# Kernel optimization log

Measured on AMD Instinct MI355X. Metric: run time of the kernel, lower is better.

Reference implementation:

```python
import jax, jax.numpy as jnp
import numpy as np

HIDDEN = 512
NUM_HEADS = 8


def setup_inputs() -> dict:
    key = jax.random.key(0)
    ks = jax.random.split(key, 8)
    Tq, Tk, Cq, Ck, H = 1, 65536, 512, 512, HIDDEN
    s = 1.0 / np.sqrt(H)
    return {
        "Q": jax.random.normal(ks[0], (Tq, Cq), jnp.float32),
        "K": jax.random.normal(ks[1], (Tk, Ck), jnp.float32),
        "Wq": jax.random.normal(ks[2], (H, Cq), jnp.float32) * s,
        "bq": jax.random.normal(ks[3], (H,), jnp.float32) * s,
        "Wk": jax.random.normal(ks[4], (H, Ck), jnp.float32) * s,
        "bk": jax.random.normal(ks[5], (H,), jnp.float32) * s,
        "Wout": jax.random.normal(ks[6], (1, NUM_HEADS), jnp.float32) * 0.3,
        "bout": jax.random.normal(ks[7], (1,), jnp.float32) * 0.3,
    }


def reference(Q, K, Wq, bq, Wk, bk, Wout, bout):
    h = NUM_HEADS
    H = Wq.shape[0]
    d = H // h  # per-head dim
    # linear + ReLU projections
    Ql = jax.nn.relu(Q @ Wq.T + bq)          # [1, H]
    Kl = jax.nn.relu(K @ Wk.T + bk)          # [Tk, H]
    # split into heads (T_q == 1 is required by linear_out)
    Qh = Ql.reshape(h, d)                    # [h, d]
    Kh = Kl.reshape(-1, h, d)                # [Tk, h, d]
    # per-head scores, scaled by sqrt(d_head); dropout rate 0 -> identity
    scores = jnp.einsum('hd,thd->th', Qh, Kh) / (d ** 0.5)  # [Tk, h]
    # learned per-head fusion, then softmax over the T_k axis
    logits = scores @ Wout.T + bout          # [Tk, 1]
    return jax.nn.softmax(logits, axis=0)    # [Tk, 1]
```

## Files before the change

kernel.cpp:

```cpp
#include <hip/hip_runtime.h>
#include <hip/hip_fp16.h>

#define CDIM 512
#define ROWS 65536
#define TPW  16

typedef _Float16 half8  __attribute__((ext_vector_type(8)));
typedef __fp16   fp16x2 __attribute__((ext_vector_type(2)));
typedef float    f32x16 __attribute__((ext_vector_type(16)));

__device__ __forceinline__ half8 cvt8(float4 f0, float4 f1) {
    union { fp16x2 h2[4]; half8 h8; } u;
    u.h2[0] = __builtin_amdgcn_cvt_pkrtz(f0.x, f0.y);
    u.h2[1] = __builtin_amdgcn_cvt_pkrtz(f0.z, f0.w);
    u.h2[2] = __builtin_amdgcn_cvt_pkrtz(f1.x, f1.y);
    u.h2[3] = __builtin_amdgcn_cvt_pkrtz(f1.z, f1.w);
    return u.h8;
}

__global__ void qproj_kernel(const float* __restrict__ Q, const float* __restrict__ Wq,
                             const float* __restrict__ bq, const float* __restrict__ Wout,
                             float* __restrict__ v) {
    __shared__ float qs[CDIM];
    const int t = threadIdx.x;
    qs[t] = Q[t]; qs[t + 256] = Q[t + 256];
    __syncthreads();
    const int jj  = t >> 4;
    const int sub = t & 15;
    const int j   = blockIdx.x * 16 + jj;
    const float4* w4 = (const float4*)(Wq + (size_t)j * CDIM + sub * 32);
    const float4* q4 = (const float4*)(qs + sub * 32);
    float s = 0.f;
    #pragma unroll
    for (int i = 0; i < 8; ++i) {
        float4 w = w4[i]; float4 q = q4[i];
        s = fmaf(w.x, q.x, s); s = fmaf(w.y, q.y, s);
        s = fmaf(w.z, q.z, s); s = fmaf(w.w, q.w, s);
    }
    s += __shfl_xor(s, 1); s += __shfl_xor(s, 2);
    s += __shfl_xor(s, 4); s += __shfl_xor(s, 8);
    if (sub == 0) {
        s += bq[j];
        s = fmaxf(s, 0.f);
        v[j] = s * Wout[j >> 6] * 0.125f;
    }
}

__global__ void wkfrag_kernel(const float* __restrict__ Wk, _Float16* __restrict__ Wkf) {
    const int gid = blockIdx.x * 256 + threadIdx.x;
    const int jb  = gid >> 11;
    const int kc  = (gid >> 6) & 31;
    const int l   = gid & 63;
    const int j   = jb * 32 + (l & 31);
    const int k   = kc * 16 + (l >> 5) * 8;
    const float* src = Wk + (size_t)j * CDIM + k;
    float4 f0 = *(const float4*)(src);
    float4 f1 = *(const float4*)(src + 4);
    *(half8*)(Wkf + (size_t)gid * 8) = cvt8(f0, f1);
}

__global__ __launch_bounds__(512, 2) void score_kernel(
    const float* __restrict__ Kmat, const _Float16* __restrict__ Wkf,
    const float* __restrict__ bk, const float* __restrict__ v,
    float* __restrict__ partial2)
{
    __shared__ alignas(16) char fragbuf[2][32768];
    __shared__ float scratch2[2][8][32];

    const int tid  = threadIdx.x;
    const int lane = tid & 63;
    const int wave = tid >> 6;
    const int l31  = lane & 31;
    const int lhi  = lane >> 5;

    const int bid      = blockIdx.x;
    const int cls      = (bid >> 3) & 1;
    const int rowblock = (bid & 7) * 16 + (bid >> 4);
    const int rowbase  = rowblock * (TPW * 32);
    const int jb       = cls * 8 + wave;
    float* pbase = partial2 + (size_t)cls * ROWS;

    half8 B[32];
    const half8* bsrc = (const half8*)Wkf + (size_t)jb * 2048 + lane;
    #pragma unroll
    for (int kc = 0; kc < 32; ++kc) B[kc] = bsrc[kc * 64];
    const int jmy = jb * 32 + l31;
    const float bj = bk[jmy];
    const float vj = v[jmy];

    const int kc0  = wave * 4;
    const int srow = tid & 31;
    const int slhi = (tid >> 5) & 1;
    const int slot = tid & 63;

    {
        const float* g0 = Kmat + (size_t)(rowbase + srow) * CDIM + kc0 * 16 + slhi * 8;
        #pragma unroll
        for (int i = 0; i < 4; ++i) {
            float4 f0 = *(const float4*)(g0 + i * 16);
            float4 f1 = *(const float4*)(g0 + i * 16 + 4);
            *(half8*)(&fragbuf[0][(kc0 + i) * 1024 + slot * 16]) = cvt8(f0, f1);
        }
    }
    __syncthreads();

    for (int t = 0; t < TPW; ++t) {
        const int cur = t & 1;
        const bool pf = (t + 1 < TPW);
        const char* sb = fragbuf[cur];
        char* db = fragbuf[cur ^ 1];
        const float* gt = Kmat + (size_t)(rowbase + (pf ? (t + 1) : t) * 32 + srow) * CDIM
                        + kc0 * 16 + slhi * 8;

        if (t > 0 && tid < 32) {
            const int pt = (t - 1) & 1;
            float s = 0.f;
            #pragma unroll
            for (int w = 0; w < 8; ++w) s += scratch2[pt][w][tid];
            pbase[rowbase + (t - 1) * 32 + tid] = s;
        }

        f32x16 acc0, acc1;
        #pragma unroll
        for (int r = 0; r < 16; ++r) { acc0[r] = 0.f; acc1[r] = 0.f; }

        float4 L0, L1, L2, L3;
        if (pf) {
            L0 = *(const float4*)(gt);
            L1 = *(const float4*)(gt + 4);
            L2 = *(const float4*)(gt + 16);
            L3 = *(const float4*)(gt + 20);
        }
        __builtin_amdgcn_sched_barrier(0);

        #pragma unroll
        for (int kc = 0; kc < 16; kc += 2) {
            half8 a0 = *(const half8*)(sb + kc * 1024 + lane * 16);
            half8 a1 = *(const half8*)(sb + (kc + 1) * 1024 + lane * 16);
            acc0 = __builtin_amdgcn_mfma_f32_32x32x16_f16(a0, B[kc],     acc0, 0, 0, 0);
            acc1 = __builtin_amdgcn_mfma_f32_32x32x16_f16(a1, B[kc + 1], acc1, 0, 0, 0);
        }

        if (pf) {
            *(half8*)(db + (kc0 + 0) * 1024 + slot * 16) = cvt8(L0, L1);
            *(half8*)(db + (kc0 + 1) * 1024 + slot * 16) = cvt8(L2, L3);
            L0 = *(const float4*)(gt + 32);
            L1 = *(const float4*)(gt + 36);
            L2 = *(const float4*)(gt + 48);
            L3 = *(const float4*)(gt + 52);
        }
        __builtin_amdgcn_sched_barrier(0);

        #pragma unroll
        for (int kc = 16; kc < 32; kc += 2) {
            half8 a0 = *(const half8*)(sb + kc * 1024 + lane * 16);
            half8 a1 = *(const half8*)(sb + (kc + 1) * 1024 + lane * 16);
            acc0 = __builtin_amdgcn_mfma_f32_32x32x16_f16(a0, B[kc],     acc0, 0, 0, 0);
            acc1 = __builtin_amdgcn_mfma_f32_32x32x16_f16(a1, B[kc + 1], acc1, 0, 0, 0);
        }

        if (pf) {
            *(half8*)(db + (kc0 + 2) * 1024 + slot * 16) = cvt8(L0, L1);
            *(half8*)(db + (kc0 + 3) * 1024 + slot * 16) = cvt8(L2, L3);
        }

        {
            float part[16];
            #pragma unroll
            for (int r = 0; r < 16; ++r)
                part[r] = fmaxf(acc0[r] + acc1[r] + bj, 0.f) * vj;

            float q0[8];
            #pragma unroll
            for (int i = 0; i < 8; ++i) {
                const bool b = lane & 1;
                float keep = b ? part[i + 8] : part[i];
                float send = b ? part[i] : part[i + 8];
                q0[i] = keep + __shfl_xor(send, 1);
            }
            float q1[4];
            #pragma unroll
            for (int i = 0; i < 4; ++i) {
                const bool b = lane & 2;
                float keep = b ? q0[i + 4] : q0[i];
                float send = b ? q0[i] : q0[i + 4];
                q1[i] = keep + __shfl_xor(send, 2);
            }
            float q2[2];
            #pragma unroll
            for (int i = 0; i < 2; ++i) {
                const bool b = lane & 4;
                float keep = b ? q1[i + 2] : q1[i];
                float send = b ? q1[i] : q1[i + 2];
                q2[i] = keep + __shfl_xor(send, 4);
            }
            float q3;
            {
                const bool b = lane & 8;
                float keep = b ? q2[1] : q2[0];
                float send = b ? q2[0] : q2[1];
                q3 = keep + __shfl_xor(send, 8);
            }
            float s = q3 + __shfl_xor(q3, 16);
            if (l31 < 16) {
                const int rr  = ((l31 & 1) << 3) | ((l31 & 2) << 1) | ((l31 & 4) >> 1) | ((l31 & 8) >> 3);
                const int row = (rr & 3) + 8 * (rr >> 2) + 4 * lhi;
                scratch2[cur][wave][row] = s;
            }
        }

        __syncthreads();
    }

    if (tid < 32) {
        const int pt = (TPW - 1) & 1;
        float s = 0.f;
        #pragma unroll
        for (int w = 0; w < 8; ++w) s += scratch2[pt][w][tid];
        pbase[rowbase + (TPW - 1) * 32 + tid] = s;
    }
}

__global__ void expsum_kernel(const float* __restrict__ partial2, float* __restrict__ logits,
                              float* __restrict__ blocksum) {
    __shared__ float red[256];
    const int t = threadIdx.x;
    const int row = blockIdx.x * 256 + t;
    const float lg = partial2[row] + partial2[ROWS + row];
    logits[row] = lg;
    red[t] = expf(lg);
    __syncthreads();
    for (int s = 128; s > 0; s >>= 1) {
        if (t < s) red[t] += red[t + s];
        __syncthreads();
    }
    if (t == 0) blocksum[blockIdx.x] = red[0];
}

__global__ void norm_kernel(const float* __restrict__ logits, const float* __restrict__ blocksum,
                            float* __restrict__ out) {
    __shared__ float red[256];
    const int t = threadIdx.x;
    red[t] = blocksum[t];
    __syncthreads();
    for (int s = 128; s > 0; s >>= 1) {
        if (t < s) red[t] += red[t + s];
        __syncthreads();
    }
    const float zinv = 1.0f / red[0];
    const int i = blockIdx.x * 256 + t;
    out[i] = expf(logits[i]) * zinv;
}

extern "C" void kernel_launch(void* const* d_in, const int* in_sizes, int n_in,
                              void* d_out, int out_size, void* d_ws, size_t ws_size,
                              hipStream_t stream) {
    const float* Q    = (const float*)d_in[0];
    const float* Kmat = (const float*)d_in[1];
    const float* Wq   = (const float*)d_in[2];
    const float* bq   = (const float*)d_in[3];
    const float* Wk   = (const float*)d_in[4];
    const float* bk   = (const float*)d_in[5];
    const float* Wout = (const float*)d_in[6];
    float* out = (float*)d_out;

    char* ws = (char*)d_ws;
    _Float16* Wkf   = (_Float16*)(ws);
    float* v        = (float*)(ws + 524288);
    float* partial2 = (float*)(ws + 526336);
    float* logits   = (float*)(ws + 1050624);
    float* blocksum = (float*)(ws + 1312768);

    hipLaunchKernelGGL(qproj_kernel,  dim3(32),   dim3(256), 0, stream, Q, Wq, bq, Wout, v);
    hipLaunchKernelGGL(wkfrag_kernel, dim3(128),  dim3(256), 0, stream, Wk, Wkf);
    hipLaunchKernelGGL(score_kernel,  dim3(256),  dim3(512), 0, stream, Kmat, Wkf, bk, v, partial2);
    hipLaunchKernelGGL(expsum_kernel, dim3(256),  dim3(256), 0, stream, partial2, logits, blocksum);
    hipLaunchKernelGGL(norm_kernel,   dim3(256),  dim3(256), 0, stream, logits, blocksum, out);
}
```

Baseline: 62.86 us.

## Merge prep kernels and give each score wave two column blocks

Combines the Q-projection and Wk fragment conversion into one launch, removing a kernel launch. The score kernel drops from 8 waves of 512 threads to 4 waves of 256, and each wave now holds two B fragment sets (64 half8 registers). Each A fragment read from LDS therefore feeds two MFMAs, halving LDS reads per MFMA. The K-tile prefetch is restructured into four quarter stages with double-buffered registers. The cost is much higher register pressure, fewer waves per block and one block per SM, which reduces latency hiding for the global K loads.

After: 61.90 us. About the same (-1.5%).

```diff
diff --git a/kernel.cpp b/kernel.cpp
--- a/kernel.cpp
+++ b/kernel.cpp
@@ -18,54 +18,55 @@
     return u.h8;
 }
 
-__global__ void qproj_kernel(const float* __restrict__ Q, const float* __restrict__ Wq,
-                             const float* __restrict__ bq, const float* __restrict__ Wout,
-                             float* __restrict__ v) {
+__global__ void prep_kernel(const float* __restrict__ Q, const float* __restrict__ Wq,
+                            const float* __restrict__ bq, const float* __restrict__ Wout,
+                            const float* __restrict__ Wk,
+                            float* __restrict__ v, _Float16* __restrict__ Wkf) {
     __shared__ float qs[CDIM];
     const int t = threadIdx.x;
-    qs[t] = Q[t]; qs[t + 256] = Q[t + 256];
-    __syncthreads();
-    const int jj  = t >> 4;
-    const int sub = t & 15;
-    const int j   = blockIdx.x * 16 + jj;
-    const float4* w4 = (const float4*)(Wq + (size_t)j * CDIM + sub * 32);
-    const float4* q4 = (const float4*)(qs + sub * 32);
-    float s = 0.f;
-    #pragma unroll
-    for (int i = 0; i < 8; ++i) {
-        float4 w = w4[i]; float4 q = q4[i];
-        s = fmaf(w.x, q.x, s); s = fmaf(w.y, q.y, s);
-        s = fmaf(w.z, q.z, s); s = fmaf(w.w, q.w, s);
-    }
-    s += __shfl_xor(s, 1); s += __shfl_xor(s, 2);
-    s += __shfl_xor(s, 4); s += __shfl_xor(s, 8);
-    if (sub == 0) {
-        s += bq[j];
-        s = fmaxf(s, 0.f);
-        v[j] = s * Wout[j >> 6] * 0.125f;
-    }
-}
-
-__global__ void wkfrag_kernel(const float* __restrict__ Wk, _Float16* __restrict__ Wkf) {
-    const int gid = blockIdx.x * 256 + threadIdx.x;
-    const int jb  = gid >> 11;
-    const int kc  = (gid >> 6) & 31;
-    const int l   = gid & 63;
-    const int j   = jb * 32 + (l & 31);
-    const int k   = kc * 16 + (l >> 5) * 8;
-    const float* src = Wk + (size_t)j * CDIM + k;
-    float4 f0 = *(const float4*)(src);
-    float4 f1 = *(const float4*)(src + 4);
-    *(half8*)(Wkf + (size_t)gid * 8) = cvt8(f0, f1);
-}
-
-__global__ __launch_bounds__(512, 2) void score_kernel(
+    if (blockIdx.x < 32) {
+        qs[t] = Q[t]; qs[t + 256] = Q[t + 256];
+        __syncthreads();
+        const int jj  = t >> 4;
+        const int sub = t & 15;
+        const int j   = blockIdx.x * 16 + jj;
+        const float4* w4 = (const float4*)(Wq + (size_t)j * CDIM + sub * 32);
+        const float4* q4 = (const float4*)(qs + sub * 32);
+        float s = 0.f;
+        #pragma unroll
+        for (int i = 0; i < 8; ++i) {
+            float4 w = w4[i]; float4 q = q4[i];
+            s = fmaf(w.x, q.x, s); s = fmaf(w.y, q.y, s);
+            s = fmaf(w.z, q.z, s); s = fmaf(w.w, q.w, s);
+        }
+        s += __shfl_xor(s, 1); s += __shfl_xor(s, 2);
+        s += __shfl_xor(s, 4); s += __shfl_xor(s, 8);
+        if (sub == 0) {
+            s += bq[j];
+            s = fmaxf(s, 0.f);
+            v[j] = s * Wout[j >> 6] * 0.125f;
+        }
+    } else {
+        const int gid = (blockIdx.x - 32) * 256 + t;
+        const int jb  = gid >> 11;
+        const int kc  = (gid >> 6) & 31;
+        const int l   = gid & 63;
+        const int j   = jb * 32 + (l & 31);
+        const int k   = kc * 16 + (l >> 5) * 8;
+        const float* src = Wk + (size_t)j * CDIM + k;
+        float4 f0 = *(const float4*)(src);
+        float4 f1 = *(const float4*)(src + 4);
+        *(half8*)(Wkf + (size_t)gid * 8) = cvt8(f0, f1);
+    }
+}
+
+__global__ __launch_bounds__(256, 1) void score_kernel(
     const float* __restrict__ Kmat, const _Float16* __restrict__ Wkf,
     const float* __restrict__ bk, const float* __restrict__ v,
     float* __restrict__ partial2)
 {
     __shared__ alignas(16) char fragbuf[2][32768];
-    __shared__ float scratch2[2][8][32];
+    __shared__ float scratch2[2][4][32];
 
     const int tid  = threadIdx.x;
     const int lane = tid & 63;
@@ -77,30 +78,44 @@
     const int cls      = (bid >> 3) & 1;
     const int rowblock = (bid & 7) * 16 + (bid >> 4);
     const int rowbase  = rowblock * (TPW * 32);
-    const int jb       = cls * 8 + wave;
     float* pbase = partial2 + (size_t)cls * ROWS;
 
-    half8 B[32];
-    const half8* bsrc = (const half8*)Wkf + (size_t)jb * 2048 + lane;
-    #pragma unroll
-    for (int kc = 0; kc < 32; ++kc) B[kc] = bsrc[kc * 64];
-    const int jmy = jb * 32 + l31;
-    const float bj = bk[jmy];
-    const float vj = v[jmy];
-
-    const int kc0  = wave * 4;
-    const int srow = tid & 31;
-    const int slhi = (tid >> 5) & 1;
-    const int slot = tid & 63;
-
+    half8 B0[32], B1[32];
     {
-        const float* g0 = Kmat + (size_t)(rowbase + srow) * CDIM + kc0 * 16 + slhi * 8;
-        #pragma unroll
-        for (int i = 0; i < 4; ++i) {
-            float4 f0 = *(const float4*)(g0 + i * 16);
-            float4 f1 = *(const float4*)(g0 + i * 16 + 4);
-            *(half8*)(&fragbuf[0][(kc0 + i) * 1024 + slot * 16]) = cvt8(f0, f1);
-        }
+        const half8* b0 = (const half8*)Wkf + (size_t)(cls * 8 + wave) * 2048 + lane;
+        const half8* b1 = (const half8*)Wkf + (size_t)(cls * 8 + 4 + wave) * 2048 + lane;
+        #pragma unroll
+        for (int kc = 0; kc < 32; ++kc) { B0[kc] = b0[kc * 64]; B1[kc] = b1[kc * 64]; }
+    }
+    const int j0 = (cls * 8 + wave) * 32 + l31;
+    const int j1 = (cls * 8 + 4 + wave) * 32 + l31;
+    const float bj0 = bk[j0], vj0 = v[j0];
+    const float bj1 = bk[j1], vj1 = v[j1];
+
+    const int srow = lane & 31;
+    const int skof = (lane >> 5) * 8;
+
+    {
+        const float* g0 = Kmat + (size_t)(rowbase + srow) * CDIM + skof;
+        #pragma unroll
+        for (int q = 0; q < 4; ++q) {
+            #pragma unroll
+            for (int h = 0; h < 2; ++h) {
+                const int kc = q * 8 + h * 4 + wave;
+                float4 f0 = *(const float4*)(g0 + kc * 16);
+                float4 f1 = *(const float4*)(g0 + kc * 16 + 4);
+                *(half8*)(&fragbuf[0][kc * 1024 + lane * 16]) = cvt8(f0, f1);
+            }
+        }
+    }
+
+    float4 L[2][4];
+    {
+        const float* g1 = Kmat + (size_t)(rowbase + 32 + srow) * CDIM + skof;
+        L[0][0] = *(const float4*)(g1 + wave * 16);
+        L[0][1] = *(const float4*)(g1 + wave * 16 + 4);
+        L[0][2] = *(const float4*)(g1 + (4 + wave) * 16);
+        L[0][3] = *(const float4*)(g1 + (4 + wave) * 16 + 4);
     }
     __syncthreads();
 
@@ -109,14 +124,12 @@
         const bool pf = (t + 1 < TPW);
         const char* sb = fragbuf[cur];
         char* db = fragbuf[cur ^ 1];
-        const float* gt = Kmat + (size_t)(rowbase + (pf ? (t + 1) : t) * 32 + srow) * CDIM
-                        + kc0 * 16 + slhi * 8;
+        const float* gt = Kmat + (size_t)(rowbase + (t + 1) * 32 + srow) * CDIM + skof;
 
         if (t > 0 && tid < 32) {
             const int pt = (t - 1) & 1;
-            float s = 0.f;
-            #pragma unroll
-            for (int w = 0; w < 8; ++w) s += scratch2[pt][w][tid];
+            float s = scratch2[pt][0][tid] + scratch2[pt][1][tid]
+                    + scratch2[pt][2][tid] + scratch2[pt][3][tid];
             pbase[rowbase + (t - 1) * 32 + tid] = s;
         }
 
@@ -124,51 +137,47 @@
         #pragma unroll
         for (int r = 0; r < 16; ++r) { acc0[r] = 0.f; acc1[r] = 0.f; }
 
-        float4 L0, L1, L2, L3;
-        if (pf) {
-            L0 = *(const float4*)(gt);
-            L1 = *(const float4*)(gt + 4);
-            L2 = *(const float4*)(gt + 16);
-            L3 = *(const float4*)(gt + 20);
+        #pragma unroll
+        for (int q = 0; q < 4; ++q) {
+            if (pf && q < 3) {
+                const int kcA = (q + 1) * 8 + wave;
+                const int kcB = (q + 1) * 8 + 4 + wave;
+                L[(q + 1) & 1][0] = *(const float4*)(gt + kcA * 16);
+                L[(q + 1) & 1][1] = *(const float4*)(gt + kcA * 16 + 4);
+                L[(q + 1) & 1][2] = *(const float4*)(gt + kcB * 16);
+                L[(q + 1) & 1][3] = *(const float4*)(gt + kcB * 16 + 4);
+            }
+            __builtin_amdgcn_sched_barrier(0);
+            #pragma unroll
+            for (int i = 0; i < 8; ++i) {
+                const int kc = q * 8 + i;
+                half8 a = *(const half8*)(sb + kc * 1024 + lane * 16);
+                acc0 = __builtin_amdgcn_mfma_f32_32x32x16_f16(a, B0[kc], acc0, 0, 0, 0);
+                acc1 = __builtin_amdgcn_mfma_f32_32x32x16_f16(a, B1[kc], acc1, 0, 0, 0);
+            }
+            if (pf) {
+                const int kcA = q * 8 + wave;
+                const int kcB = q * 8 + 4 + wave;
+                *(half8*)(db + kcA * 1024 + lane * 16) = cvt8(L[q & 1][0], L[q & 1][1]);
+                *(half8*)(db + kcB * 1024 + lane * 16) = cvt8(L[q & 1][2], L[q & 1][3]);
+            }
+            __builtin_amdgcn_sched_barrier(0);
+        }
+
+        if (t + 2 < TPW) {
+            const float* gn = gt + 32 * CDIM;
+            L[0][0] = *(const float4*)(gn + wave * 16);
+            L[0][1] = *(const float4*)(gn + wave * 16 + 4);
+            L[0][2] = *(const float4*)(gn + (4 + wave) * 16);
+            L[0][3] = *(const float4*)(gn + (4 + wave) * 16 + 4);
         }
         __builtin_amdgcn_sched_barrier(0);
-
-        #pragma unroll
-        for (int kc = 0; kc < 16; kc += 2) {
-            half8 a0 = *(const half8*)(sb + kc * 1024 + lane * 16);
-            half8 a1 = *(const half8*)(sb + (kc + 1) * 1024 + lane * 16);
-            acc0 = __builtin_amdgcn_mfma_f32_32x32x16_f16(a0, B[kc],     acc0, 0, 0, 0);
-            acc1 = __builtin_amdgcn_mfma_f32_32x32x16_f16(a1, B[kc + 1], acc1, 0, 0, 0);
-        }
-
-        if (pf) {
-            *(half8*)(db + (kc0 + 0) * 1024 + slot * 16) = cvt8(L0, L1);
-            *(half8*)(db + (kc0 + 1) * 1024 + slot * 16) = cvt8(L2, L3);
-            L0 = *(const float4*)(gt + 32);
-            L1 = *(const float4*)(gt + 36);
-            L2 = *(const float4*)(gt + 48);
-            L3 = *(const float4*)(gt + 52);
-        }
-        __builtin_amdgcn_sched_barrier(0);
-
-        #pragma unroll
-        for (int kc = 16; kc < 32; kc += 2) {
-            half8 a0 = *(const half8*)(sb + kc * 1024 + lane * 16);
-            half8 a1 = *(const half8*)(sb + (kc + 1) * 1024 + lane * 16);
-            acc0 = __builtin_amdgcn_mfma_f32_32x32x16_f16(a0, B[kc],     acc0, 0, 0, 0);
-            acc1 = __builtin_amdgcn_mfma_f32_32x32x16_f16(a1, B[kc + 1], acc1, 0, 0, 0);
-        }
-
-        if (pf) {
-            *(half8*)(db + (kc0 + 2) * 1024 + slot * 16) = cvt8(L0, L1);
-            *(half8*)(db + (kc0 + 3) * 1024 + slot * 16) = cvt8(L2, L3);
-        }
 
         {
             float part[16];
             #pragma unroll
             for (int r = 0; r < 16; ++r)
-                part[r] = fmaxf(acc0[r] + acc1[r] + bj, 0.f) * vj;
+                part[r] = fmaxf(acc0[r] + bj0, 0.f) * vj0 + fmaxf(acc1[r] + bj1, 0.f) * vj1;
 
             float q0[8];
             #pragma unroll
@@ -214,9 +223,8 @@
 
     if (tid < 32) {
         const int pt = (TPW - 1) & 1;
-        float s = 0.f;
-        #pragma unroll
-        for (int w = 0; w < 8; ++w) s += scratch2[pt][w][tid];
+        float s = scratch2[pt][0][tid] + scratch2[pt][1][tid]
+                + scratch2[pt][2][tid] + scratch2[pt][3][tid];
         pbase[rowbase + (TPW - 1) * 32 + tid] = s;
     }
 }
@@ -271,9 +279,8 @@
     float* logits   = (float*)(ws + 1050624);
     float* blocksum = (float*)(ws + 1312768);
 
-    hipLaunchKernelGGL(qproj_kernel,  dim3(32),   dim3(256), 0, stream, Q, Wq, bq, Wout, v);
-    hipLaunchKernelGGL(wkfrag_kernel, dim3(128),  dim3(256), 0, stream, Wk, Wkf);
-    hipLaunchKernelGGL(score_kernel,  dim3(256),  dim3(512), 0, stream, Kmat, Wkf, bk, v, partial2);
+    hipLaunchKernelGGL(prep_kernel,   dim3(160),  dim3(256), 0, stream, Q, Wq, bq, Wout, Wk, v, Wkf);
+    hipLaunchKernelGGL(score_kernel,  dim3(256),  dim3(256), 0, stream, Kmat, Wkf, bk, v, partial2);
     hipLaunchKernelGGL(expsum_kernel, dim3(256),  dim3(256), 0, stream, partial2, logits, blocksum);
     hipLaunchKernelGGL(norm_kernel,   dim3(256),  dim3(256), 0, stream, logits, blocksum, out);
 }
```
